# Performance work log

Hardware: AMD Instinct MI355X
Metric: run time of the kernel (lower is better)

The kernel has to match this reference:

```python
import jax, jax.numpy as jnp
import numpy as np

B, T, H = 32, 512, 1024   # batch, seq, hidden
L = 512                   # max_seq_length (must be <= 512 for rel_pos_bias)
E = 2048                  # hidden * expansion_factor
S = 128                   # shared qk dim
SQRT_S = float(np.sqrt(S))
EPS = 1e-5


def setup_inputs() -> dict:
    key = jax.random.key(0)
    ks = jax.random.split(key, 9)
    return {
        "x": jax.random.normal(ks[0], (B, T, H), jnp.float32),
        "ln_w": jnp.ones((H,), jnp.float32),
        "ln_b": jnp.zeros((H,), jnp.float32),
        "uv_w": jax.random.normal(ks[1], (2 * E + S, H), jnp.float32) * 0.02,  # torch Linear [out,in]
        "uv_b": jnp.zeros((2 * E + S,), jnp.float32),
        "gamma": jax.random.uniform(ks[2], (2, S), jnp.float32),
        "beta": jax.random.uniform(ks[3], (2, S), jnp.float32),
        "w": jax.random.uniform(ks[4], (2 * L - 1,), jnp.float32),  # Toeplitz rel-pos table
        "o_w": jax.random.normal(ks[5], (H, E), jnp.float32) * 0.02,
        "o_b": jnp.zeros((H,), jnp.float32),
    }


def _rope(x):
    # x: [B, T, 2, S]; positions run along the seq dim (dim=1), faithful to GAU.rope
    half = x.shape[-1] // 2
    pos = jnp.arange(x.shape[1], dtype=x.dtype)
    # note: original uses 10000**(+i/half) (increasing freq) — keep it faithful
    inv_freq = 10000.0 ** (jnp.arange(half, dtype=x.dtype) / half)
    sinusoid = pos[:, None] * inv_freq[None, :]          # [T, half]
    sin = jnp.sin(sinusoid)[None, :, None, :]            # [1, T, 1, half]
    cos = jnp.cos(sinusoid)[None, :, None, :]
    x1, x2 = jnp.split(x, 2, axis=-1)
    return jnp.concatenate([x1 * cos - x2 * sin, x2 * cos + x1 * sin], axis=-1)


def reference(x, ln_w, ln_b, uv_w, uv_b, gamma, beta, w, o_w, o_b):
    Tq = x.shape[1]
    shortcut = x  # hidden_size == output_size -> residual
    # LayerNorm
    mu = jnp.mean(x, axis=-1, keepdims=True)
    var = jnp.mean(jnp.square(x - mu), axis=-1, keepdims=True)
    xn = (x - mu) / jnp.sqrt(var + EPS) * ln_w + ln_b
    # fused uv projection + SiLU, then split into gate u, value v, base
    uv = jax.nn.silu(xn @ uv_w.T + uv_b)                  # [B, T, 2E+S]
    u, v, base = uv[..., :E], uv[..., E:2 * E], uv[..., 2 * E:]
    base = base[:, :, None, :] * gamma[None, None] + beta  # [B, T, 2, S]
    base = _rope(base)
    q, k = base[:, :, 0, :], base[:, :, 1, :]             # [B, T, S]
    qk = jnp.einsum('bis,bjs->bij', q, k)                 # [B, T, T]
    # Toeplitz rel-pos bias: bias[i, j] = w[j - i + L - 1]
    rel = jnp.arange(Tq)[None, :] - jnp.arange(Tq)[:, None] + (L - 1)
    bias = w[rel]                                         # [T, T]
    kernel = jnp.square(jax.nn.relu(qk / SQRT_S + bias[None]))  # squared-ReLU attention
    out = u * jnp.einsum('bij,bje->bie', kernel, v)       # gated attention output [B, T, E]
    return out @ o_w.T + o_b + shortcut
```

## Files before the change

### kernel.cpp

```cpp
#include <hip/hip_runtime.h>

typedef unsigned short u16;
typedef __bf16 bf16x8 __attribute__((ext_vector_type(8)));
typedef float f32x4 __attribute__((ext_vector_type(4)));

#define B_ 32
#define T_ 512
#define H_ 1024
#define E_ 2048
#define S_ 128

__device__ inline u16 f2bf(float f) {
  union { float f; unsigned int u; } c; c.f = f;
  unsigned int u = c.u;
  unsigned int r = (u + 0x7FFFu + ((u >> 16) & 1u)) >> 16;
  return (u16)r;
}
__device__ inline float bf2f(u16 h) {
  union { unsigned int u; float f; } c; c.u = ((unsigned int)h) << 16; return c.f;
}
__device__ inline float silu_fast(float v) {
  return v * __builtin_amdgcn_rcpf(1.0f + __expf(-v));
}

__device__ inline void g2lds16(const u16* g, u16* l) {
  __builtin_amdgcn_global_load_lds(
      (const __attribute__((address_space(1))) void*)g,
      (__attribute__((address_space(3))) void*)l, 16, 0, 0);
}

__global__ __launch_bounds__(256) void ln_kernel(const float* __restrict__ x,
                                                 const float* __restrict__ lw,
                                                 const float* __restrict__ lb,
                                                 u16* __restrict__ xn) {
  int row = blockIdx.x;
  int t = threadIdx.x;
  const float4* xr = (const float4*)(x + (size_t)row * H_);
  float4 v = xr[t];
  float s = v.x + v.y + v.z + v.w;
  float ss = v.x * v.x + v.y * v.y + v.z * v.z + v.w * v.w;
  for (int off = 1; off < 64; off <<= 1) {
    s += __shfl_xor(s, off);
    ss += __shfl_xor(ss, off);
  }
  __shared__ float red[8];
  int w = t >> 6, l = t & 63;
  if (l == 0) { red[w] = s; red[4 + w] = ss; }
  __syncthreads();
  s = red[0] + red[1] + red[2] + red[3];
  ss = red[4] + red[5] + red[6] + red[7];
  float mu = s * (1.0f / H_);
  float var = ss * (1.0f / H_) - mu * mu;
  float inv = rsqrtf(var + 1e-5f);
  int i = t * 4;
  ushort4 o;
  o.x = f2bf((v.x - mu) * inv * lw[i] + lb[i]);
  o.y = f2bf((v.y - mu) * inv * lw[i + 1] + lb[i + 1]);
  o.z = f2bf((v.z - mu) * inv * lw[i + 2] + lb[i + 2]);
  o.w = f2bf((v.w - mu) * inv * lw[i + 3] + lb[i + 3]);
  *(ushort4*)(xn + (size_t)row * H_ + i) = o;
}

__global__ void cvt_kernel(const float* __restrict__ in, u16* __restrict__ out, int n4) {
  int i = blockIdx.x * 256 + threadIdx.x;
  if (i < n4) {
    float4 v = ((const float4*)in)[i];
    ushort4 o;
    o.x = f2bf(v.x); o.y = f2bf(v.y); o.z = f2bf(v.z); o.w = f2bf(v.w);
    ((ushort4*)out)[i] = o;
  }
}

__global__ __launch_bounds__(256) void rope_kernel(const float* __restrict__ base,
                                                   const float* __restrict__ gamma,
                                                   const float* __restrict__ beta,
                                                   u16* __restrict__ q,
                                                   u16* __restrict__ k) {
  int row = blockIdx.x * 4 + (threadIdx.x >> 6);
  int s = threadIdx.x & 63;
  int t = row & (T_ - 1);
  const float* bp = base + (size_t)row * S_;
  float b1 = bp[s], b2 = bp[s + 64];
  float q1 = b1 * gamma[s] + beta[s];
  float q2 = b2 * gamma[64 + s] + beta[64 + s];
  float k1 = b1 * gamma[128 + s] + beta[128 + s];
  float k2 = b2 * gamma[192 + s] + beta[192 + s];
  float invf = (float)pow(10000.0, (double)s * (1.0 / 64.0));
  float ph = (float)t * invf;
  float sn, cs;
  sincosf(ph, &sn, &cs);
  size_t o = (size_t)row * S_;
  q[o + s]      = f2bf(q1 * cs - q2 * sn);
  q[o + 64 + s] = f2bf(q2 * cs + q1 * sn);
  k[o + s]      = f2bf(k1 * cs - k2 * sn);
  k[o + 64 + s] = f2bf(k2 * cs + k1 * sn);
}

template <int MODE>
__global__ __launch_bounds__(256)
void gemm_bt(const u16* __restrict__ A, const u16* __restrict__ Bm,
             int K, long long sA, long long sB,
             void* __restrict__ o0, void* __restrict__ o1, void* __restrict__ o2,
             const void* __restrict__ c0, const void* __restrict__ c1, int nb0) {
  __shared__ __attribute__((aligned(16))) u16 lds[32768];
  u16* lsA = lds;
  u16* lsB = lds + 16384;

  const int z = blockIdx.z;
  const u16* Ab = A + (long long)z * sA;
  const u16* Bb = Bm + (long long)z * sB;
  const int m0 = blockIdx.y * 128;
  const int n0 = nb0 + blockIdx.x * 128;
  const int t = threadIdx.x;
  const int w = t >> 6, l = t & 63;
  const int quad = l >> 4, l16 = l & 15;
  const int wm = (w >> 1) * 64, wn = (w & 1) * 64;
  const int srow = t >> 4;
  const int gl = (t & 15) ^ ((t >> 4) & 7);
  const int dst_off = t * 8;
  const int rsw = l16 & 7;

  f32x4 zero = {0.f, 0.f, 0.f, 0.f};
  f32x4 acc[4][4];
  for (int mi = 0; mi < 4; ++mi)
    for (int ni = 0; ni < 4; ++ni) acc[mi][ni] = zero;

  const u16* gA = Ab + ((size_t)(m0 + srow) * K + gl * 8);
  const u16* gB = Bb + ((size_t)(n0 + srow) * K + gl * 8);
  const size_t rK16 = (size_t)16 * K;

  for (int k0 = 0; k0 < K; k0 += 128) {
    __syncthreads();
#pragma unroll
    for (int c = 0; c < 8; ++c)
      g2lds16(gA + k0 + c * rK16, &lsA[c * 2048 + dst_off]);
#pragma unroll
    for (int c = 0; c < 8; ++c)
      g2lds16(gB + k0 + c * rK16, &lsB[c * 2048 + dst_off]);
    __syncthreads();
#pragma unroll
    for (int j = 0; j < 4; ++j) {
      int pg = ((j * 4 + quad) ^ rsw) * 8;
      bf16x8 af[4], bfr[4];
      for (int i = 0; i < 4; ++i) {
        af[i]  = *(const bf16x8*)&lsA[(wm + i * 16 + l16) * 128 + pg];
        bfr[i] = *(const bf16x8*)&lsB[(wn + i * 16 + l16) * 128 + pg];
      }
      for (int mi = 0; mi < 4; ++mi)
        for (int ni = 0; ni < 4; ++ni)
          acc[mi][ni] = __builtin_amdgcn_mfma_f32_16x16x32_bf16(af[mi], bfr[ni], acc[mi][ni], 0, 0, 0);
    }
  }

  if constexpr (MODE == 0) {
    const float* uvb = (const float*)c0;
    if (n0 < E_) {
      for (int mi = 0; mi < 4; ++mi)
        for (int ni = 0; ni < 4; ++ni) {
          int n = n0 + wn + ni * 16 + l16;
          float bias = uvb[n];
          for (int r = 0; r < 4; ++r) {
            int m = m0 + wm + mi * 16 + quad * 4 + r;
            ((u16*)o0)[(size_t)m * E_ + n] = f2bf(silu_fast(acc[mi][ni][r] + bias));
          }
        }
    } else if (n0 < 2 * E_) {
      const int bb = m0 >> 9;
      const int tt0 = m0 & (T_ - 1);
      const int nv0 = n0 - E_;
      for (int h = 0; h < 2; ++h) {
        __syncthreads();
        if ((w & 1) == h) {
          for (int mi = 0; mi < 4; ++mi)
            for (int ni = 0; ni < 4; ++ni) {
              int nl = ni * 16 + l16;
              float bias = uvb[n0 + h * 64 + nl];
              for (int r = 0; r < 4; ++r) {
                int ml = wm + mi * 16 + quad * 4 + r;
                u16 sv = f2bf(silu_fast(acc[mi][ni][r] + bias));
                int g = ml >> 3, o = ml & 7;
                int gs = g ^ (nl & 7);
                lds[nl * 128 + gs * 8 + o] = sv;
              }
            }
        }
        __syncthreads();
        int row = t >> 2;
        int q4 = t & 3;
        size_t gbase = ((size_t)bb * E_ + nv0 + h * 64 + row) * T_ + tt0;
        for (int gg = 0; gg < 4; ++gg) {
          int g = q4 * 4 + gg;
          int gsw = g ^ (row & 7);
          uint4 val = *(const uint4*)&lds[row * 128 + gsw * 8];
          *(uint4*)&(((u16*)o1)[gbase + g * 8]) = val;
        }
      }
    } else {
      for (int mi = 0; mi < 4; ++mi)
        for (int ni = 0; ni < 4; ++ni) {
          int n = n0 + wn + ni * 16 + l16;
          float bias = uvb[n];
          for (int r = 0; r < 4; ++r) {
            int m = m0 + wm + mi * 16 + quad * 4 + r;
            ((float*)o2)[(size_t)m * S_ + (n - 2 * E_)] = silu_fast(acc[mi][ni][r] + bias);
          }
        }
    }
  } else {
    for (int mi = 0; mi < 4; ++mi) {
      for (int ni = 0; ni < 4; ++ni) {
        int n = n0 + wn + ni * 16 + l16;
        for (int r = 0; r < 4; ++r) {
          int m = m0 + wm + mi * 16 + quad * 4 + r;
          float a = acc[mi][ni][r];
          if constexpr (MODE == 1) {
            const float* wrel = (const float*)c0;
            float v = a * 0.08838834764831845f + wrel[n - m + 511];
            v = fmaxf(v, 0.0f);
            ((u16*)o0)[(size_t)z * (T_ * T_) + (size_t)m * T_ + n] = f2bf(v * v);
          } else if constexpr (MODE == 2) {
            const u16* uu = (const u16*)c0;
            size_t gi = ((size_t)z * T_ + m) * E_ + n;
            float uv_ = bf2f(uu[gi]);
            ((u16*)o0)[gi] = f2bf(a * uv_);
          } else {
            const float* ob = (const float*)c0;
            const float* xs = (const float*)c1;
            size_t gi = (size_t)m * H_ + n;
            ((float*)o0)[gi] = a + ob[n] + xs[gi];
          }
        }
      }
    }
  }
}

#define PH_SYNC()                                        \
  asm volatile("s_waitcnt lgkmcnt(0)" ::: "memory");     \
  __builtin_amdgcn_sched_barrier(0);                     \
  __builtin_amdgcn_s_barrier();                          \
  __builtin_amdgcn_sched_barrier(0);                     \
  __builtin_amdgcn_s_setprio(1);

#define PH_END()                                         \
  __builtin_amdgcn_s_setprio(0);

#define MM4(mb)                                                                                                   \
  _Pragma("unroll")                                                                                               \
  for (int ni = 0; ni < 4; ++ni) {                                                                                \
    acc[mb + 0][ni] = __builtin_amdgcn_mfma_f32_16x16x32_bf16(af[mb + 0][0], bfr[ni][0], acc[mb + 0][ni], 0, 0, 0); \
    acc[mb + 1][ni] = __builtin_amdgcn_mfma_f32_16x16x32_bf16(af[mb + 1][0], bfr[ni][0], acc[mb + 1][ni], 0, 0, 0); \
    acc[mb + 2][ni] = __builtin_amdgcn_mfma_f32_16x16x32_bf16(af[mb + 2][0], bfr[ni][0], acc[mb + 2][ni], 0, 0, 0); \
    acc[mb + 3][ni] = __builtin_amdgcn_mfma_f32_16x16x32_bf16(af[mb + 3][0], bfr[ni][0], acc[mb + 3][ni], 0, 0, 0); \
  }                                                                                                               \
  _Pragma("unroll")                                                                                               \
  for (int ni = 0; ni < 4; ++ni) {                                                                                \
    acc[mb + 0][ni] = __builtin_amdgcn_mfma_f32_16x16x32_bf16(af[mb + 0][1], bfr[ni][1], acc[mb + 0][ni], 0, 0, 0); \
    acc[mb + 1][ni] = __builtin_amdgcn_mfma_f32_16x16x32_bf16(af[mb + 1][1], bfr[ni][1], acc[mb + 1][ni], 0, 0, 0); \
    acc[mb + 2][ni] = __builtin_amdgcn_mfma_f32_16x16x32_bf16(af[mb + 2][1], bfr[ni][1], acc[mb + 2][ni], 0, 0, 0); \
    acc[mb + 3][ni] = __builtin_amdgcn_mfma_f32_16x16x32_bf16(af[mb + 3][1], bfr[ni][1], acc[mb + 3][ni], 0, 0, 0); \
  }

template <int MODE, bool XSWZ>
__global__ __launch_bounds__(512, 2)
void gemm256(const u16* __restrict__ A, const u16* __restrict__ Bm,
             int K, long long sA, long long sB,
             void* __restrict__ o0, void* __restrict__ o1,
             const void* __restrict__ c0, const void* __restrict__ c1) {
  extern __shared__ u16 lds[];

  int bx = blockIdx.x, by = blockIdx.y;
  if constexpr (XSWZ) {
    int gx = gridDim.x;
    int nwg = gx * gridDim.y;
    int hh = by * gx + bx;
    int cpx = nwg >> 3;
    int lid = (hh & 7) * cpx + (hh >> 3);
    bx = lid % gx; by = lid / gx;
  }
  const int z = blockIdx.z;
  const u16* Ab = A + (long long)z * sA;
  const u16* Bb = Bm + (long long)z * sB;
  const int m0 = by * 256;
  const int n0 = bx * 256;
  const int t = threadIdx.x;
  const int w = t >> 6, ln = t & 63;
  const int quad = ln >> 4, l16 = ln & 15;
  const int wm = w >> 2, wn = w & 3;

  const int nkt = K >> 6;

  const int goff = ((t & 7) ^ ((t >> 3) & 7)) * 8;
  const u16* gA = Ab + (size_t)(m0 + (t >> 3)) * K + goff;
  const u16* gB = Bb + (size_t)(n0 + (t >> 3)) * K + goff;
  u16* ldst = lds + t * 8;
  const size_t rK64 = (size_t)64 * K;
  const size_t rK128 = (size_t)128 * K;

  auto SA = [&](int b, int h, int kt) {
    const u16* g = gA + h * rK128 + (size_t)kt * 64;
    u16* d = ldst + b * 16384 + h * 8192;
    g2lds16(g, d);
    g2lds16(g + rK64, d + 4096);
  };
  auto SB = [&](int b, int h, int kt) {
    const u16* g = gB + h * rK128 + (size_t)kt * 64;
    u16* d = ldst + 32768 + b * 16384 + h * 8192;
    g2lds16(g, d);
    g2lds16(g + rK64, d + 4096);
  };

  f32x4 zero = {0.f, 0.f, 0.f, 0.f};
  f32x4 acc[8][4];
#pragma unroll
  for (int mi = 0; mi < 8; ++mi)
#pragma unroll
    for (int ni = 0; ni < 4; ++ni) acc[mi][ni] = zero;

  SA(0, 0, 0); SA(0, 1, 0); SB(0, 0, 0); SB(0, 1, 0);
  if (nkt > 1) {
    SB(1, 0, 1); SB(1, 1, 1);
    asm volatile("s_waitcnt vmcnt(4)" ::: "memory");
  } else {
    asm volatile("s_waitcnt vmcnt(0)" ::: "memory");
  }
  __builtin_amdgcn_s_barrier();

  const u16* lA0 = lds + wm * 8192 + l16 * 64;
  const u16* lB0 = lds + 32768 + (wn >> 1) * 8192 + ((wn & 1) * 64 + l16) * 64;
  const int pg0 = (quad ^ (l16 & 7)) * 8;
  const int pg1 = ((4 + quad) ^ (l16 & 7)) * 8;

  bf16x8 bfr[4][2];
  bf16x8 af[8][2];

  for (int j = 0; j < nkt; ++j) {
    const int b = j & 1;
    const u16* lA = lA0 + b * 16384;
    const u16* lB = lB0 + b * 16384;

#pragma unroll
    for (int ni = 0; ni < 4; ++ni) {
      bfr[ni][0] = *(const bf16x8*)&lB[ni * 1024 + pg0];
      bfr[ni][1] = *(const bf16x8*)&lB[ni * 1024 + pg1];
    }
#pragma unroll
    for (int mi = 0; mi < 4; ++mi) {
      af[mi][0] = *(const bf16x8*)&lA[mi * 1024 + pg0];
      af[mi][1] = *(const bf16x8*)&lA[mi * 1024 + pg1];
    }
    if (j + 1 < nkt) { SA(b ^ 1, 0, j + 1); SA(b ^ 1, 1, j + 1); }
    PH_SYNC();
    MM4(0);
    PH_END();

#pragma unroll
    for (int mi = 4; mi < 8; ++mi) {
      af[mi][0] = *(const bf16x8*)&lA[mi * 1024 + pg0];
      af[mi][1] = *(const bf16x8*)&lA[mi * 1024 + pg1];
    }
    if (j + 2 < nkt) {
      SB(b, 0, j + 2); SB(b, 1, j + 2);
      asm volatile("s_waitcnt lgkmcnt(0)" ::: "memory");
      asm volatile("s_waitcnt vmcnt(4)" ::: "memory");
    } else {
      asm volatile("s_waitcnt lgkmcnt(0)" ::: "memory");
      asm volatile("s_waitcnt vmcnt(0)" ::: "memory");
    }
    __builtin_amdgcn_sched_barrier(0);
    __builtin_amdgcn_s_barrier();
    __builtin_amdgcn_sched_barrier(0);
    __builtin_amdgcn_s_setprio(1);
    MM4(4);
    PH_END();
  }

  if constexpr (MODE == 0) {
    const float* uvb = (const float*)c0;
    if (n0 < E_) {
#pragma unroll
      for (int ni = 0; ni < 4; ++ni) {
        int n = n0 + wn * 64 + ni * 16 + l16;
        float bias = uvb[n];
#pragma unroll
        for (int mi = 0; mi < 8; ++mi)
#pragma unroll
          for (int r = 0; r < 4; ++r) {
            int m = m0 + wm * 128 + mi * 16 + quad * 4 + r;
            ((u16*)o0)[(size_t)m * E_ + n] = f2bf(silu_fast(acc[mi][ni][r] + bias));
          }
      }
    } else {
      const int bb = m0 >> 9;
      const int tt0 = m0 & (T_ - 1);
      const int nv0 = n0 - E_;
#pragma unroll
      for (int ni = 0; ni < 4; ++ni) {
        int nl = wn * 64 + ni * 16 + l16;
        float bias = uvb[n0 + nl];
#pragma unroll
        for (int mi = 0; mi < 8; ++mi)
#pragma unroll
          for (int r = 0; r < 4; ++r) {
            int ml = wm * 128 + mi * 16 + quad * 4 + r;
            u16 sv = f2bf(silu_fast(acc[mi][ni][r] + bias));
            int g = ml >> 3, o = ml & 7;
            lds[nl * 256 + ((g ^ (nl & 7)) << 3) + o] = sv;
          }
      }
      __syncthreads();
      int row = t >> 1;
      u16* o1p = (u16*)o1;
      size_t gbase = ((size_t)bb * E_ + nv0 + row) * T_ + tt0;
#pragma unroll
      for (int cc = 0; cc < 16; ++cc) {
        int c = (t & 1) * 16 + cc;
        int gs = c ^ (row & 7);
        uint4 val = *(const uint4*)&lds[row * 256 + gs * 8];
        *(uint4*)&o1p[gbase + c * 8] = val;
      }
    }
  } else if constexpr (MODE == 2) {
    const u16* uu = (const u16*)c0;
#pragma unroll
    for (int mi = 0; mi < 8; ++mi)
#pragma unroll
      for (int ni = 0; ni < 4; ++ni) {
        int n = n0 + wn * 64 + ni * 16 + l16;
#pragma unroll
        for (int r = 0; r < 4; ++r) {
          int m = m0 + wm * 128 + mi * 16 + quad * 4 + r;
          size_t gi = ((size_t)z * T_ + m) * E_ + n;
          float uv_ = bf2f(uu[gi]);
          ((u16*)o0)[gi] = f2bf(acc[mi][ni][r] * uv_);
        }
      }
  } else {
    const float* ob = (const float*)c0;
    const float* xs = (const float*)c1;
#pragma unroll
    for (int ni = 0; ni < 4; ++ni) {
      int n = n0 + wn * 64 + ni * 16 + l16;
      float bias = ob[n];
#pragma unroll
      for (int mi = 0; mi < 8; ++mi)
#pragma unroll
        for (int r = 0; r < 4; ++r) {
          int m = m0 + wm * 128 + mi * 16 + quad * 4 + r;
          size_t gi = (size_t)m * H_ + n;
          ((float*)o0)[gi] = acc[mi][ni][r] + bias + xs[gi];
        }
    }
  }
}

extern "C" void kernel_launch(void* const* d_in, const int* in_sizes, int n_in,
                              void* d_out, int out_size, void* d_ws, size_t ws_size,
                              hipStream_t stream) {
  const float* x     = (const float*)d_in[0];
  const float* ln_w  = (const float*)d_in[1];
  const float* ln_b  = (const float*)d_in[2];
  const float* uv_w  = (const float*)d_in[3];
  const float* uv_b  = (const float*)d_in[4];
  const float* gamma = (const float*)d_in[5];
  const float* beta  = (const float*)d_in[6];
  const float* wrel  = (const float*)d_in[7];
  const float* o_w   = (const float*)d_in[8];
  const float* o_b   = (const float*)d_in[9];

  char* ws = (char*)d_ws;
  u16*   xn   = (u16*)(ws);
  u16*   qb   = (u16*)(ws);
  u16*   kb   = (u16*)(ws + 4194304);
  u16*   km   = (u16*)(ws + 8388608);
  u16*   uvwb = (u16*)(ws + 33554432);
  u16*   owb  = (u16*)(ws + 42205184);
  u16*   u    = (u16*)(ws + 46399488);
  u16*   vt   = (u16*)(ws + 113508352);
  float* base = (float*)(ws + 180617216);
  u16*   attn = u;

  static int use256 = -1;
  if (use256 < 0) {
    auto* k0 = gemm256<0, true>;
    auto* k2 = gemm256<2, false>;
    auto* k3 = gemm256<3, true>;
    hipError_t e0 = hipFuncSetAttribute((const void*)k0, hipFuncAttributeMaxDynamicSharedMemorySize, 131072);
    hipError_t e2 = hipFuncSetAttribute((const void*)k2, hipFuncAttributeMaxDynamicSharedMemorySize, 131072);
    hipError_t e3 = hipFuncSetAttribute((const void*)k3, hipFuncAttributeMaxDynamicSharedMemorySize, 131072);
    use256 = (e0 == hipSuccess && e2 == hipSuccess && e3 == hipSuccess) ? 1 : 0;
  }

  ln_kernel<<<16384, 256, 0, stream>>>(x, ln_w, ln_b, xn);
  cvt_kernel<<<4224, 256, 0, stream>>>(uv_w, uvwb, 4224 * 1024 / 4);
  cvt_kernel<<<2048, 256, 0, stream>>>(o_w, owb, 1024 * 2048 / 4);

  if (use256) {
    gemm256<0, true><<<dim3(16, 64, 1), 512, 131072, stream>>>(
        xn, uvwb, 1024, 0, 0, u, vt, uv_b, nullptr);
    gemm_bt<0><<<dim3(1, 128, 1), 256, 0, stream>>>(
        xn, uvwb, 1024, 0, 0, u, vt, base, uv_b, nullptr, 4096);
    rope_kernel<<<4096, 256, 0, stream>>>(base, gamma, beta, qb, kb);
    gemm_bt<1><<<dim3(4, 4, 32), 256, 0, stream>>>(
        qb, kb, 128, 65536, 65536, km, nullptr, nullptr, wrel, nullptr, 0);
    gemm256<2, false><<<dim3(8, 2, 32), 512, 131072, stream>>>(
        km, vt, 512, 262144, 1048576, attn, nullptr, u, nullptr);
    gemm256<3, true><<<dim3(4, 64, 1), 512, 131072, stream>>>(
        attn, owb, 2048, 0, 0, d_out, nullptr, o_b, x);
  } else {
    gemm_bt<0><<<dim3(33, 128, 1), 256, 0, stream>>>(
        xn, uvwb, 1024, 0, 0, u, vt, base, uv_b, nullptr, 0);
    rope_kernel<<<4096, 256, 0, stream>>>(base, gamma, beta, qb, kb);
    gemm_bt<1><<<dim3(4, 4, 32), 256, 0, stream>>>(
        qb, kb, 128, 65536, 65536, km, nullptr, nullptr, wrel, nullptr, 0);
    gemm_bt<2><<<dim3(16, 4, 32), 256, 0, stream>>>(
        km, vt, 512, 262144, 1048576, attn, nullptr, nullptr, u, nullptr, 0);
    gemm_bt<3><<<dim3(8, 128, 1), 256, 0, stream>>>(
        attn, owb, 2048, 0, 0, d_out, nullptr, nullptr, o_b, x, 0);
  }
}
```

Measured before the change: 528.5 us.

## Replace 256x256 GEMM with 256x128 tile, 4 waves, triple-buffered K=32 pipeline

The 512-thread 256x256-tile GEMM becomes a 256-thread 256x128-tile kernel. It uses K-steps of 32, three LDS stages with prefetch two steps ahead, and a single barrier per step. The MODE 0 transpose epilogue now writes the V^T tile in two 64-column halves through LDS. LDS drops from 128KB to 72KB per block and the grid doubles along N, aiming for better occupancy and wave balance. In exchange there is less data reuse per tile, and the fallback path that checked whether the attribute call succeeded is removed.

```diff
diff --git a/kernel.cpp b/kernel.cpp
--- a/kernel.cpp
+++ b/kernel.cpp
@@ -235,35 +235,9 @@
   }
 }
 
-#define PH_SYNC()                                        \
-  asm volatile("s_waitcnt lgkmcnt(0)" ::: "memory");     \
-  __builtin_amdgcn_sched_barrier(0);                     \
-  __builtin_amdgcn_s_barrier();                          \
-  __builtin_amdgcn_sched_barrier(0);                     \
-  __builtin_amdgcn_s_setprio(1);
-
-#define PH_END()                                         \
-  __builtin_amdgcn_s_setprio(0);
-
-#define MM4(mb)                                                                                                   \
-  _Pragma("unroll")                                                                                               \
-  for (int ni = 0; ni < 4; ++ni) {                                                                                \
-    acc[mb + 0][ni] = __builtin_amdgcn_mfma_f32_16x16x32_bf16(af[mb + 0][0], bfr[ni][0], acc[mb + 0][ni], 0, 0, 0); \
-    acc[mb + 1][ni] = __builtin_amdgcn_mfma_f32_16x16x32_bf16(af[mb + 1][0], bfr[ni][0], acc[mb + 1][ni], 0, 0, 0); \
-    acc[mb + 2][ni] = __builtin_amdgcn_mfma_f32_16x16x32_bf16(af[mb + 2][0], bfr[ni][0], acc[mb + 2][ni], 0, 0, 0); \
-    acc[mb + 3][ni] = __builtin_amdgcn_mfma_f32_16x16x32_bf16(af[mb + 3][0], bfr[ni][0], acc[mb + 3][ni], 0, 0, 0); \
-  }                                                                                                               \
-  _Pragma("unroll")                                                                                               \
-  for (int ni = 0; ni < 4; ++ni) {                                                                                \
-    acc[mb + 0][ni] = __builtin_amdgcn_mfma_f32_16x16x32_bf16(af[mb + 0][1], bfr[ni][1], acc[mb + 0][ni], 0, 0, 0); \
-    acc[mb + 1][ni] = __builtin_amdgcn_mfma_f32_16x16x32_bf16(af[mb + 1][1], bfr[ni][1], acc[mb + 1][ni], 0, 0, 0); \
-    acc[mb + 2][ni] = __builtin_amdgcn_mfma_f32_16x16x32_bf16(af[mb + 2][1], bfr[ni][1], acc[mb + 2][ni], 0, 0, 0); \
-    acc[mb + 3][ni] = __builtin_amdgcn_mfma_f32_16x16x32_bf16(af[mb + 3][1], bfr[ni][1], acc[mb + 3][ni], 0, 0, 0); \
-  }
-
 template <int MODE, bool XSWZ>
-__global__ __launch_bounds__(512, 2)
-void gemm256(const u16* __restrict__ A, const u16* __restrict__ Bm,
+__global__ __launch_bounds__(256, 2)
+void gemm_bn(const u16* __restrict__ A, const u16* __restrict__ Bm,
              int K, long long sA, long long sB,
              void* __restrict__ o0, void* __restrict__ o1,
              const void* __restrict__ c0, const void* __restrict__ c1) {
@@ -282,32 +256,32 @@
   const u16* Ab = A + (long long)z * sA;
   const u16* Bb = Bm + (long long)z * sB;
   const int m0 = by * 256;
-  const int n0 = bx * 256;
+  const int n0 = bx * 128;
   const int t = threadIdx.x;
   const int w = t >> 6, ln = t & 63;
   const int quad = ln >> 4, l16 = ln & 15;
-  const int wm = w >> 2, wn = w & 3;
-
-  const int nkt = K >> 6;
-
-  const int goff = ((t & 7) ^ ((t >> 3) & 7)) * 8;
-  const u16* gA = Ab + (size_t)(m0 + (t >> 3)) * K + goff;
-  const u16* gB = Bb + (size_t)(n0 + (t >> 3)) * K + goff;
+  const int wm = w >> 1, wn = w & 1;
+
+  const int nkt = K >> 5;
+
+  const int srow = t >> 2;
+  const int goff = ((t & 3) ^ ((t >> 3) & 3)) * 8;
+  const u16* gA = Ab + (size_t)(m0 + srow) * K + goff;
+  const u16* gB = Bb + (size_t)(n0 + srow) * K + goff;
   u16* ldst = lds + t * 8;
   const size_t rK64 = (size_t)64 * K;
-  const size_t rK128 = (size_t)128 * K;
-
-  auto SA = [&](int b, int h, int kt) {
-    const u16* g = gA + h * rK128 + (size_t)kt * 64;
-    u16* d = ldst + b * 16384 + h * 8192;
-    g2lds16(g, d);
-    g2lds16(g + rK64, d + 4096);
+
+  auto SA = [&](int b, int j) {
+    const u16* g = gA + (size_t)j * 32;
+    u16* d = ldst + b * 12288;
+#pragma unroll
+    for (int q = 0; q < 4; ++q) g2lds16(g + q * rK64, d + q * 2048);
   };
-  auto SB = [&](int b, int h, int kt) {
-    const u16* g = gB + h * rK128 + (size_t)kt * 64;
-    u16* d = ldst + 32768 + b * 16384 + h * 8192;
-    g2lds16(g, d);
-    g2lds16(g + rK64, d + 4096);
+  auto SB = [&](int b, int j) {
+    const u16* g = gB + (size_t)j * 32;
+    u16* d = ldst + b * 12288 + 8192;
+#pragma unroll
+    for (int q = 0; q < 2; ++q) g2lds16(g + q * rK64, d + q * 2048);
   };
 
   f32x4 zero = {0.f, 0.f, 0.f, 0.f};
@@ -317,52 +291,34 @@
 #pragma unroll
     for (int ni = 0; ni < 4; ++ni) acc[mi][ni] = zero;
 
-  SA(0, 0, 0); SA(0, 1, 0); SB(0, 0, 0); SB(0, 1, 0);
-  if (nkt > 1) {
-    SB(1, 0, 1); SB(1, 1, 1);
-    asm volatile("s_waitcnt vmcnt(4)" ::: "memory");
-  } else {
-    asm volatile("s_waitcnt vmcnt(0)" ::: "memory");
-  }
+  SA(0, 0); SB(0, 0);
+  SA(1, 1); SB(1, 1);
+  asm volatile("s_waitcnt vmcnt(6)" ::: "memory");
   __builtin_amdgcn_s_barrier();
 
-  const u16* lA0 = lds + wm * 8192 + l16 * 64;
-  const u16* lB0 = lds + 32768 + (wn >> 1) * 8192 + ((wn & 1) * 64 + l16) * 64;
-  const int pg0 = (quad ^ (l16 & 7)) * 8;
-  const int pg1 = ((4 + quad) ^ (l16 & 7)) * 8;
-
-  bf16x8 bfr[4][2];
-  bf16x8 af[8][2];
-
+  const u16* lA0 = lds + (wm * 128 + l16) * 32;
+  const u16* lB0 = lds + 8192 + (wn * 64 + l16) * 32;
+  const int pg = (quad ^ ((l16 >> 1) & 3)) * 8;
+
+  bf16x8 af[8];
+  bf16x8 bfr[4];
+
+  int b = 0, b2 = 2;
   for (int j = 0; j < nkt; ++j) {
-    const int b = j & 1;
-    const u16* lA = lA0 + b * 16384;
-    const u16* lB = lB0 + b * 16384;
-
-#pragma unroll
-    for (int ni = 0; ni < 4; ++ni) {
-      bfr[ni][0] = *(const bf16x8*)&lB[ni * 1024 + pg0];
-      bfr[ni][1] = *(const bf16x8*)&lB[ni * 1024 + pg1];
-    }
-#pragma unroll
-    for (int mi = 0; mi < 4; ++mi) {
-      af[mi][0] = *(const bf16x8*)&lA[mi * 1024 + pg0];
-      af[mi][1] = *(const bf16x8*)&lA[mi * 1024 + pg1];
-    }
-    if (j + 1 < nkt) { SA(b ^ 1, 0, j + 1); SA(b ^ 1, 1, j + 1); }
-    PH_SYNC();
-    MM4(0);
-    PH_END();
-
-#pragma unroll
-    for (int mi = 4; mi < 8; ++mi) {
-      af[mi][0] = *(const bf16x8*)&lA[mi * 1024 + pg0];
-      af[mi][1] = *(const bf16x8*)&lA[mi * 1024 + pg1];
-    }
+    const u16* lA = lA0 + b * 12288;
+    const u16* lB = lB0 + b * 12288;
+
+#pragma unroll
+    for (int ni = 0; ni < 4; ++ni)
+      bfr[ni] = *(const bf16x8*)&lB[ni * 512 + pg];
+#pragma unroll
+    for (int mi = 0; mi < 8; ++mi)
+      af[mi] = *(const bf16x8*)&lA[mi * 512 + pg];
+
     if (j + 2 < nkt) {
-      SB(b, 0, j + 2); SB(b, 1, j + 2);
+      SA(b2, j + 2); SB(b2, j + 2);
       asm volatile("s_waitcnt lgkmcnt(0)" ::: "memory");
-      asm volatile("s_waitcnt vmcnt(4)" ::: "memory");
+      asm volatile("s_waitcnt vmcnt(6)" ::: "memory");
     } else {
       asm volatile("s_waitcnt lgkmcnt(0)" ::: "memory");
       asm volatile("s_waitcnt vmcnt(0)" ::: "memory");
@@ -370,9 +326,17 @@
     __builtin_amdgcn_sched_barrier(0);
     __builtin_amdgcn_s_barrier();
     __builtin_amdgcn_sched_barrier(0);
+
     __builtin_amdgcn_s_setprio(1);
-    MM4(4);
-    PH_END();
+#pragma unroll
+    for (int ni = 0; ni < 4; ++ni)
+#pragma unroll
+      for (int mi = 0; mi < 8; ++mi)
+        acc[mi][ni] = __builtin_amdgcn_mfma_f32_16x16x32_bf16(af[mi], bfr[ni], acc[mi][ni], 0, 0, 0);
+    __builtin_amdgcn_s_setprio(0);
+
+    b = (b == 2) ? 0 : b + 1;
+    b2 = (b2 == 2) ? 0 : b2 + 1;
   }
 
   if constexpr (MODE == 0) {
@@ -394,30 +358,37 @@
       const int bb = m0 >> 9;
       const int tt0 = m0 & (T_ - 1);
       const int nv0 = n0 - E_;
-#pragma unroll
-      for (int ni = 0; ni < 4; ++ni) {
-        int nl = wn * 64 + ni * 16 + l16;
-        float bias = uvb[n0 + nl];
-#pragma unroll
-        for (int mi = 0; mi < 8; ++mi)
-#pragma unroll
-          for (int r = 0; r < 4; ++r) {
-            int ml = wm * 128 + mi * 16 + quad * 4 + r;
-            u16 sv = f2bf(silu_fast(acc[mi][ni][r] + bias));
-            int g = ml >> 3, o = ml & 7;
-            lds[nl * 256 + ((g ^ (nl & 7)) << 3) + o] = sv;
+      u16* o1p = (u16*)o1;
+#pragma unroll
+      for (int h = 0; h < 2; ++h) {
+        __syncthreads();
+        if (wn == h) {
+#pragma unroll
+          for (int ni = 0; ni < 4; ++ni) {
+            int nl = ni * 16 + l16;
+            float bias = uvb[n0 + h * 64 + nl];
+#pragma unroll
+            for (int mi = 0; mi < 8; ++mi)
+#pragma unroll
+              for (int r = 0; r < 4; ++r) {
+                int ml = wm * 128 + mi * 16 + quad * 4 + r;
+                u16 sv = f2bf(silu_fast(acc[mi][ni][r] + bias));
+                int g = ml >> 3, o = ml & 7;
+                lds[nl * 256 + ((g ^ (nl & 7)) << 3) + o] = sv;
+              }
           }
-      }
-      __syncthreads();
-      int row = t >> 1;
-      u16* o1p = (u16*)o1;
-      size_t gbase = ((size_t)bb * E_ + nv0 + row) * T_ + tt0;
-#pragma unroll
-      for (int cc = 0; cc < 16; ++cc) {
-        int c = (t & 1) * 16 + cc;
-        int gs = c ^ (row & 7);
-        uint4 val = *(const uint4*)&lds[row * 256 + gs * 8];
-        *(uint4*)&o1p[gbase + c * 8] = val;
+        }
+        __syncthreads();
+        int row = t >> 2;
+        int c0i = (t & 3) * 8;
+        size_t gbase = ((size_t)bb * E_ + nv0 + h * 64 + row) * T_ + tt0;
+#pragma unroll
+        for (int cc = 0; cc < 8; ++cc) {
+          int c = c0i + cc;
+          int gs = c ^ (row & 7);
+          uint4 val = *(const uint4*)&lds[row * 256 + gs * 8];
+          *(uint4*)&o1p[gbase + c * 8] = val;
+        }
       }
     }
   } else if constexpr (MODE == 2) {
@@ -480,42 +451,30 @@
   float* base = (float*)(ws + 180617216);
   u16*   attn = u;
 
-  static int use256 = -1;
-  if (use256 < 0) {
-    auto* k0 = gemm256<0, true>;
-    auto* k2 = gemm256<2, false>;
-    auto* k3 = gemm256<3, true>;
-    hipError_t e0 = hipFuncSetAttribute((const void*)k0, hipFuncAttributeMaxDynamicSharedMemorySize, 131072);
-    hipError_t e2 = hipFuncSetAttribute((const void*)k2, hipFuncAttributeMaxDynamicSharedMemorySize, 131072);
-    hipError_t e3 = hipFuncSetAttribute((const void*)k3, hipFuncAttributeMaxDynamicSharedMemorySize, 131072);
-    use256 = (e0 == hipSuccess && e2 == hipSuccess && e3 == hipSuccess) ? 1 : 0;
+  static int ldsset = -1;
+  if (ldsset < 0) {
+    auto* k0 = gemm_bn<0, true>;
+    auto* k2 = gemm_bn<2, false>;
+    auto* k3 = gemm_bn<3, true>;
+    hipFuncSetAttribute((const void*)k0, hipFuncAttributeMaxDynamicSharedMemorySize, 73728);
+    hipFuncSetAttribute((const void*)k2, hipFuncAttributeMaxDynamicSharedMemorySize, 73728);
+    hipFuncSetAttribute((const void*)k3, hipFuncAttributeMaxDynamicSharedMemorySize, 73728);
+    ldsset = 1;
   }
 
   ln_kernel<<<16384, 256, 0, stream>>>(x, ln_w, ln_b, xn);
   cvt_kernel<<<4224, 256, 0, stream>>>(uv_w, uvwb, 4224 * 1024 / 4);
   cvt_kernel<<<2048, 256, 0, stream>>>(o_w, owb, 1024 * 2048 / 4);
 
-  if (use256) {
-    gemm256<0, true><<<dim3(16, 64, 1), 512, 131072, stream>>>(
-        xn, uvwb, 1024, 0, 0, u, vt, uv_b, nullptr);
-    gemm_bt<0><<<dim3(1, 128, 1), 256, 0, stream>>>(
-        xn, uvwb, 1024, 0, 0, u, vt, base, uv_b, nullptr, 4096);
-    rope_kernel<<<4096, 256, 0, stream>>>(base, gamma, beta, qb, kb);
-    gemm_bt<1><<<dim3(4, 4, 32), 256, 0, stream>>>(
-        qb, kb, 128, 65536, 65536, km, nullptr, nullptr, wrel, nullptr, 0);
-    gemm256<2, false><<<dim3(8, 2, 32), 512, 131072, stream>>>(
-        km, vt, 512, 262144, 1048576, attn, nullptr, u, nullptr);
-    gemm256<3, true><<<dim3(4, 64, 1), 512, 131072, stream>>>(
-        attn, owb, 2048, 0, 0, d_out, nullptr, o_b, x);
-  } else {
-    gemm_bt<0><<<dim3(33, 128, 1), 256, 0, stream>>>(
-        xn, uvwb, 1024, 0, 0, u, vt, base, uv_b, nullptr, 0);
-    rope_kernel<<<4096, 256, 0, stream>>>(base, gamma, beta, qb, kb);
-    gemm_bt<1><<<dim3(4, 4, 32), 256, 0, stream>>>(
-        qb, kb, 128, 65536, 65536, km, nullptr, nullptr, wrel, nullptr, 0);
-    gemm_bt<2><<<dim3(16, 4, 32), 256, 0, stream>>>(
-        km, vt, 512, 262144, 1048576, attn, nullptr, nullptr, u, nullptr, 0);
-    gemm_bt<3><<<dim3(8, 128, 1), 256, 0, stream>>>(
-        attn, owb, 2048, 0, 0, d_out, nullptr, nullptr, o_b, x, 0);
-  }
-}
+  gemm_bn<0, true><<<dim3(32, 64, 1), 256, 73728, stream>>>(
+      xn, uvwb, 1024, 0, 0, u, vt, uv_b, nullptr);
+  gemm_bt<0><<<dim3(1, 128, 1), 256, 0, stream>>>(
+      xn, uvwb, 1024, 0, 0, u, vt, base, uv_b, nullptr, 4096);
+  rope_kernel<<<4096, 256, 0, stream>>>(base, gamma, beta, qb, kb);
+  gemm_bt<1><<<dim3(4, 4, 32), 256, 0, stream>>>(
+      qb, kb, 128, 65536, 65536, km, nullptr, nullptr, wrel, nullptr, 0);
+  gemm_bn<2, false><<<dim3(16, 2, 32), 256, 73728, stream>>>(
+      km, vt, 512, 262144, 1048576, attn, nullptr, u, nullptr);
+  gemm_bn<3, true><<<dim3(8, 64, 1), 256, 73728, stream>>>(
+      attn, owb, 2048, 0, 0, d_out, nullptr, o_b, x);
+}
```

After: 534.1 us. About the same (+1.1%).
